# Performance work log

Hardware: AMD Instinct MI355X
Metric: run time of the kernel (lower is better)

## Reference

```python
import jax, jax.numpy as jnp
import numpy as np

B, C, H, W = 4, 512, 64, 64
WS = 32          # window size (square)
NHEADS = 8
GROUPS = 32      # GroupNorm groups (ldm Normalize)
EPS = 1e-6


def setup_inputs() -> dict:
    key = jax.random.key(0)
    ks = jax.random.split(key, 6)
    p = lambda k: jax.random.normal(k, (C, C), jnp.float32) * 0.02
    return {
        "x": jax.random.normal(ks[0], (B, C, H, W), jnp.float32),
        "norm_scale": jnp.ones((C,), jnp.float32),
        "norm_bias": jnp.zeros((C,), jnp.float32),
        "wq": p(ks[1]), "bq": jnp.zeros((C,), jnp.float32),
        "wk": p(ks[2]), "bk": jnp.zeros((C,), jnp.float32),
        "wv": p(ks[3]), "bv": jnp.zeros((C,), jnp.float32),
        "wo": p(ks[4]), "bo": jnp.zeros((C,), jnp.float32),
    }


def _group_norm(x, scale, bias):
    b, c, h, w = x.shape
    xg = x.reshape(b, GROUPS, c // GROUPS, h, w)
    mu = xg.mean(axis=(2, 3, 4), keepdims=True)
    var = ((xg - mu) ** 2).mean(axis=(2, 3, 4), keepdims=True)
    xn = ((xg - mu) * jax.lax.rsqrt(var + EPS)).reshape(b, c, h, w)
    return xn * scale[None, :, None, None] + bias[None, :, None, None]


def _conv1x1(t, w, b):
    return jnp.einsum('bchw,oc->bohw', t, w) + b[None, :, None, None]


def reference(x, norm_scale, norm_bias, wq, bq, wk, bk, wv, bv, wo, bo):
    b, c, hh, ww = x.shape
    h_ = _group_norm(x, norm_scale, norm_bias)

    # window partition: b c (h w1) (w w2) -> (b h w) c w1 w2  (H,W divisible by WS, no pad)
    nH, nW = hh // WS, ww // WS
    h_ = h_.reshape(b, c, nH, WS, nW, WS).transpose(0, 2, 4, 1, 3, 5)
    h_ = h_.reshape(b * nH * nW, c, WS, WS)

    q = _conv1x1(h_, wq, bq)
    k = _conv1x1(h_, wk, bk)
    v = _conv1x1(h_, wv, bv)

    bw = q.shape[0]
    n = WS * WS
    d = c // NHEADS

    def to_heads(t):  # b c h w -> b heads n d
        t = t.reshape(bw, c, n).transpose(0, 2, 1)          # b n c
        return t.reshape(bw, n, NHEADS, d).transpose(0, 2, 1, 3)

    q, k, v = map(to_heads, (q, k, v))

    scale = 1.0 / jnp.sqrt(jnp.asarray(d, q.dtype))
    scores = jnp.einsum('bhnd,bhmd->bhnm', q, k) * scale    # [bw, heads, n, n]
    attn = jax.nn.softmax(scores, axis=-1)
    out = jnp.einsum('bhnm,bhmd->bhnd', attn, v)
    out = out.transpose(0, 2, 1, 3).reshape(bw, n, c)       # b n c

    # window reverse: (b h w) (w1 w2) c -> b c (h w1) (w w2)
    out = out.reshape(b, nH, nW, WS, WS, c).transpose(0, 5, 1, 3, 2, 4)
    out = out.reshape(b, c, hh, ww)

    out = _conv1x1(out, wo, bo)
    return x + out
```

## Files before the change

kernel.cpp:

```cpp
#include <hip/hip_runtime.h>
#include <math.h>

typedef __bf16 bf16_t;
typedef bf16_t bf16x8 __attribute__((ext_vector_type(8)));
typedef float f32x16 __attribute__((ext_vector_type(16)));
typedef unsigned int u32x4 __attribute__((ext_vector_type(4)));

#define MFMA32(a, b, c) __builtin_amdgcn_mfma_f32_32x32x16_bf16(a, b, c, 0, 0, 0)
#define ROWOF(r, h) (((r) & 3) + 8 * ((r) >> 2) + 4 * (h))


static constexpr size_t OFF_STATS = 0;
static constexpr size_t OFF_W     = 4096;
static constexpr size_t OFF_HT    = OFF_W + 4u * 524288u;
static constexpr size_t OFF_Q     = OFF_HT + 16777216u;
static constexpr size_t OFF_K     = OFF_Q + 16777216u;
static constexpr size_t OFF_V     = OFF_K + 16777216u;
static constexpr size_t OFF_O     = OFF_HT;

__device__ __forceinline__ unsigned short f2bf(float f) {
  unsigned int u = __float_as_uint(f);
  u += 0x7fffu + ((u >> 16) & 1u);
  return (unsigned short)(u >> 16);
}

__global__ __launch_bounds__(256) void wconv_k(const float* __restrict__ w0, const float* __restrict__ w1,
                                               const float* __restrict__ w2, const float* __restrict__ w3,
                                               unsigned short* __restrict__ dst) {
  const float* srcs[4] = {w0, w1, w2, w3};
  const float* src = srcs[blockIdx.y];
  unsigned short* d = dst + (size_t)blockIdx.y * 262144u;
  int i = (blockIdx.x * 256 + threadIdx.x) * 4;
  float4 v = *(const float4*)(src + i);
  unsigned int lo = (unsigned int)f2bf(v.x) | ((unsigned int)f2bf(v.y) << 16);
  unsigned int hi = (unsigned int)f2bf(v.z) | ((unsigned int)f2bf(v.w) << 16);
  uint2 pk; pk.x = lo; pk.y = hi;
  *(uint2*)(d + i) = pk;
}

__global__ __launch_bounds__(256) void gn_stats_k(const float* __restrict__ x, float* __restrict__ stats) {
  int bg = blockIdx.x;
  const float* p = x + (size_t)bg * 65536u;
  int t = threadIdx.x;
  float s = 0.f, ss = 0.f;
  for (int i = t * 4; i < 65536; i += 1024) {
    float4 v = *(const float4*)(p + i);
    s += v.x + v.y + v.z + v.w;
    ss += v.x * v.x + v.y * v.y + v.z * v.z + v.w * v.w;
  }
  for (int m = 1; m <= 32; m <<= 1) { s += __shfl_xor(s, m); ss += __shfl_xor(ss, m); }
  __shared__ float rs[4], rss[4];
  int wv = t >> 6;
  if ((t & 63) == 0) { rs[wv] = s; rss[wv] = ss; }
  __syncthreads();
  if (t == 0) {
    s = rs[0] + rs[1] + rs[2] + rs[3];
    ss = rss[0] + rss[1] + rss[2] + rss[3];
    float mean = s * (1.f / 65536.f);
    float var = ss * (1.f / 65536.f) - mean * mean;
    stats[bg * 2] = mean;
    stats[bg * 2 + 1] = rsqrtf(var + 1e-6f);
  }
}

__global__ __launch_bounds__(256) void gn_apply_k(const float* __restrict__ x, const float* __restrict__ scale,
                                                  const float* __restrict__ bias, const float* __restrict__ stats,
                                                  unsigned short* __restrict__ ht) {
  __shared__ float tile[64][65];
  int blk = blockIdx.x;
  int b = blk >> 9, cblk = (blk >> 6) & 7, sblk = blk & 63;
  int c0 = cblk * 64, s0 = sblk * 64;
  int t = threadIdx.x;
#pragma unroll
  for (int p = 0; p < 4; ++p) {
    int i = p * 16 + (t >> 4);
    int j = (t & 15) * 4;
    int c = c0 + i;
    float mean = stats[(b * 32 + (c >> 4)) * 2];
    float rstd = stats[(b * 32 + (c >> 4)) * 2 + 1];
    float a = rstd * scale[c];
    float b2 = bias[c] - mean * a;
    float4 v = *(const float4*)(x + ((size_t)(b * 512 + c)) * 4096u + s0 + j);
    tile[i][j + 0] = v.x * a + b2;
    tile[i][j + 1] = v.y * a + b2;
    tile[i][j + 2] = v.z * a + b2;
    tile[i][j + 3] = v.w * a + b2;
  }
  __syncthreads();
#pragma unroll
  for (int p = 0; p < 8; ++p) {
    int jj = p * 8 + (t >> 5);
    int c2 = (t & 31) * 2;
    unsigned int pk = (unsigned int)f2bf(tile[c2][jj]) | ((unsigned int)f2bf(tile[c2 + 1][jj]) << 16);
    *(unsigned int*)(ht + ((size_t)b * 4096u + s0 + jj) * 512u + c0 + c2) = pk;
  }
}

__global__ __launch_bounds__(256, 2) void qkv_gemm_k(const unsigned short* __restrict__ wbf,
                                                     const unsigned short* __restrict__ ht,
                                                     const float* __restrict__ bq, const float* __restrict__ bk,
                                                     const float* __restrict__ bv,
                                                     unsigned short* __restrict__ Qatt,
                                                     unsigned short* __restrict__ Katt,
                                                     unsigned short* __restrict__ Vt) {
  int proj = blockIdx.z >> 2, b = blockIdx.z & 3;
  const unsigned short* W = wbf + (size_t)proj * 262144u;
  const float* biasp = (proj == 0) ? bq : (proj == 1) ? bk : bv;
  int o0 = blockIdx.x * 128, s0 = blockIdx.y * 128;
  __shared__ unsigned short Wl[128 * 72];
  __shared__ unsigned short Xl[128 * 72];
  int t = threadIdx.x, lane = t & 63, wv = t >> 6;
  int col_l = lane & 31, half = lane >> 5;
  int qm = (wv >> 1) * 64, qn = (wv & 1) * 64;
  f32x16 acc[2][2];
#pragma unroll
  for (int i = 0; i < 2; i++)
#pragma unroll
    for (int j = 0; j < 2; j++)
#pragma unroll
      for (int r = 0; r < 16; r++) acc[i][j][r] = 0.f;

  const unsigned short* hb = ht + ((size_t)b * 4096u + s0) * 512u;
  for (int kb = 0; kb < 512; kb += 64) {
    __syncthreads();
    {
      int row = t >> 3, ch = (t & 7) * 8;
#pragma unroll
      for (int p = 0; p < 4; ++p, row += 32) {
        *(uint4*)(Wl + row * 72 + ch) = *(const uint4*)(W + (size_t)(o0 + row) * 512u + kb + ch);
        *(uint4*)(Xl + row * 72 + ch) = *(const uint4*)(hb + (size_t)row * 512u + kb + ch);
      }
    }
    __syncthreads();
    const unsigned short* aT = (proj == 2) ? Wl : Xl;
    const unsigned short* bT = (proj == 2) ? Xl : Wl;
#pragma unroll
    for (int ks = 0; ks < 64; ks += 16) {
      bf16x8 a0 = *(const bf16x8*)(aT + (qm + col_l) * 72 + ks + 8 * half);
      bf16x8 a1 = *(const bf16x8*)(aT + (qm + 32 + col_l) * 72 + ks + 8 * half);
      bf16x8 b0 = *(const bf16x8*)(bT + (qn + col_l) * 72 + ks + 8 * half);
      bf16x8 b1 = *(const bf16x8*)(bT + (qn + 32 + col_l) * 72 + ks + 8 * half);
      acc[0][0] = MFMA32(a0, b0, acc[0][0]);
      acc[0][1] = MFMA32(a0, b1, acc[0][1]);
      acc[1][0] = MFMA32(a1, b0, acc[1][0]);
      acc[1][1] = MFMA32(a1, b1, acc[1][1]);
    }
  }

  if (proj <= 1) {
    unsigned short* dst = (proj == 0) ? Qatt : Katt;
#pragma unroll
    for (int i = 0; i < 2; i++)
#pragma unroll
      for (int j = 0; j < 2; j++) {
        int o = o0 + qn + 32 * j + col_l;
        int head = o >> 6, dd = o & 63;
        float bb = biasp[o];
#pragma unroll
        for (int r = 0; r < 16; r++) {
          int s = s0 + qm + 32 * i + ROWOF(r, half);
          int h = s >> 6, w = s & 63;
          int win = b * 4 + (h >> 5) * 2 + (w >> 5);
          int n = ((h & 31) << 5) | (w & 31);
          dst[(((size_t)(win * 8 + head)) * 1024u + n) * 64u + dd] = f2bf(acc[i][j][r] + bb);
        }
      }
  } else {
#pragma unroll
    for (int i = 0; i < 2; i++)
#pragma unroll
      for (int j = 0; j < 2; j++) {
        int s = s0 + qn + 32 * j + col_l;
        int h = s >> 6, w = s & 63;
        int win = b * 4 + (h >> 5) * 2 + (w >> 5);
        int n = ((h & 31) << 5) | (w & 31);
#pragma unroll
        for (int r = 0; r < 16; r++) {
          int o = o0 + qm + 32 * i + ROWOF(r, half);
          int head = o >> 6, dd = o & 63;
          Vt[(((size_t)(win * 8 + head)) * 64u + dd) * 1024u + n] = f2bf(acc[i][j][r] + biasp[o]);
        }
      }
  }
}

__global__ __launch_bounds__(256, 3) void attn_k(const unsigned short* __restrict__ Qatt,
                                                 const unsigned short* __restrict__ Katt,
                                                 const unsigned short* __restrict__ Vt,
                                                 unsigned short* __restrict__ Oimg) {
  int rb = blockIdx.x, head = blockIdx.y, win = blockIdx.z;
  int t = threadIdx.x, lane = t & 63, wv = t >> 6;
  int col_l = lane & 31, half = lane >> 5;
  __shared__ unsigned short Kl[128 * 72];
  __shared__ unsigned short Vl[64 * 136];
  const size_t wh = (size_t)(win * 8 + head);
  const unsigned short* Qb = Qatt + wh * 65536u;
  const unsigned short* Kb = Katt + wh * 65536u;
  const unsigned short* Vb = Vt + wh * 65536u;

  int qrow = rb * 128 + wv * 32 + col_l;
  bf16x8 qf[4];
#pragma unroll
  for (int kk = 0; kk < 4; kk++) qf[kk] = *(const bf16x8*)(Qb + (size_t)qrow * 64u + kk * 16 + 8 * half);

  f32x16 oacc[2];
#pragma unroll
  for (int j = 0; j < 2; j++)
#pragma unroll
    for (int r = 0; r < 16; r++) oacc[j][r] = 0.f;
  float lsum = 0.f;

  const float SC = 0.125f * 1.44269504f;

  for (int kt = 0; kt < 8; ++kt) {
    __syncthreads();
    {
      int row = t >> 3, ch = (t & 7) * 8;
#pragma unroll
      for (int p = 0; p < 4; ++p, row += 32)
        *(uint4*)(Kl + row * 72 + ch) = *(const uint4*)(Kb + ((size_t)(kt * 128 + row)) * 64u + ch);
      int vrow = t >> 4, vch = (t & 15) * 8;
#pragma unroll
      for (int p = 0; p < 4; ++p, vrow += 16)
        *(uint4*)(Vl + vrow * 136 + vch) = *(const uint4*)(Vb + (size_t)vrow * 1024u + kt * 128 + vch);
    }
    __syncthreads();

    f32x16 sacc[4];
#pragma unroll
    for (int jb = 0; jb < 4; jb++)
#pragma unroll
      for (int r = 0; r < 16; r++) sacc[jb][r] = 0.f;
#pragma unroll
    for (int jb = 0; jb < 4; jb++) {
#pragma unroll
      for (int kk = 0; kk < 4; kk++) {
        bf16x8 af = *(const bf16x8*)(Kl + (jb * 32 + col_l) * 72 + kk * 16 + 8 * half);
        sacc[jb] = MFMA32(af, qf[kk], sacc[jb]);
      }
    }

#pragma unroll
    for (int jb = 0; jb < 4; jb++) {
      float p[16];
#pragma unroll
      for (int r = 0; r < 16; r++) p[r] = __builtin_amdgcn_exp2f(sacc[jb][r] * SC);
      float ps = ((p[0] + p[1]) + (p[2] + p[3])) + ((p[4] + p[5]) + (p[6] + p[7]));
      ps += ((p[8] + p[9]) + (p[10] + p[11])) + ((p[12] + p[13]) + (p[14] + p[15]));
      lsum += ps;
      unsigned int pk[8];
#pragma unroll
      for (int j = 0; j < 8; j++)
        pk[j] = __builtin_amdgcn_perm(__float_as_uint(p[2 * j + 1]), __float_as_uint(p[2 * j]), 0x07060302u);
      unsigned int rA = __shfl_xor((int)(half ? pk[0] : pk[2]), 32);
      unsigned int rB = __shfl_xor((int)(half ? pk[1] : pk[3]), 32);
      unsigned int rC = __shfl_xor((int)(half ? pk[4] : pk[6]), 32);
      unsigned int rD = __shfl_xor((int)(half ? pk[5] : pk[7]), 32);
      u32x4 f0, f1;
      f0[0] = half ? rA : pk[0];
      f0[1] = half ? rB : pk[1];
      f0[2] = half ? pk[2] : rA;
      f0[3] = half ? pk[3] : rB;
      f1[0] = half ? rC : pk[4];
      f1[1] = half ? rD : pk[5];
      f1[2] = half ? pk[6] : rC;
      f1[3] = half ? pk[7] : rD;
      bf16x8 pa0 = __builtin_bit_cast(bf16x8, f0);
      bf16x8 pa1 = __builtin_bit_cast(bf16x8, f1);
#pragma unroll
      for (int dblk = 0; dblk < 2; dblk++) {
        bf16x8 v0 = *(const bf16x8*)(Vl + (dblk * 32 + col_l) * 136 + (jb * 2 + 0) * 16 + 8 * half);
        bf16x8 v1 = *(const bf16x8*)(Vl + (dblk * 32 + col_l) * 136 + (jb * 2 + 1) * 16 + 8 * half);
        oacc[dblk] = MFMA32(pa0, v0, oacc[dblk]);
        oacc[dblk] = MFMA32(pa1, v1, oacc[dblk]);
      }
    }
  }

  float l = lsum + __shfl_xor(lsum, 32);
  float inv = 1.f / l;

  int b = win >> 2, whn = (win >> 1) & 1, wwn = win & 1;
#pragma unroll
  for (int r = 0; r < 16; r++) {
    int qr = ROWOF(r, half);
    float invr = __shfl(inv, qr);
    int ntok = rb * 128 + wv * 32 + qr;
    int h = whn * 32 + (ntok >> 5), w = wwn * 32 + (ntok & 31);
    int s = h * 64 + w;
    size_t rowbase = ((size_t)b * 4096u + s) * 512u + head * 64;
    Oimg[rowbase + col_l] = f2bf(oacc[0][r] * invr);
    Oimg[rowbase + 32 + col_l] = f2bf(oacc[1][r] * invr);
  }
}

__global__ __launch_bounds__(256, 2) void out_gemm_k(const unsigned short* __restrict__ wo_bf,
                                                     const unsigned short* __restrict__ Oimg,
                                                     const float* __restrict__ bo, const float* __restrict__ x,
                                                     float* __restrict__ out) {
  int b = blockIdx.z;
  int o0 = blockIdx.x * 128, s0 = blockIdx.y * 128;
  __shared__ unsigned short Wl[128 * 72];
  __shared__ unsigned short Xl[128 * 72];
  int t = threadIdx.x, lane = t & 63, wv = t >> 6;
  int col_l = lane & 31, half = lane >> 5;
  int qm = (wv >> 1) * 64, qn = (wv & 1) * 64;
  f32x16 acc[2][2];
#pragma unroll
  for (int i = 0; i < 2; i++)
#pragma unroll
    for (int j = 0; j < 2; j++)
#pragma unroll
      for (int r = 0; r < 16; r++) acc[i][j][r] = 0.f;

  const unsigned short* ob = Oimg + ((size_t)b * 4096u + s0) * 512u;
  for (int kb = 0; kb < 512; kb += 64) {
    __syncthreads();
    {
      int row = t >> 3, ch = (t & 7) * 8;
#pragma unroll
      for (int p = 0; p < 4; ++p, row += 32) {
        *(uint4*)(Wl + row * 72 + ch) = *(const uint4*)(wo_bf + (size_t)(o0 + row) * 512u + kb + ch);
        *(uint4*)(Xl + row * 72 + ch) = *(const uint4*)(ob + (size_t)row * 512u + kb + ch);
      }
    }
    __syncthreads();
#pragma unroll
    for (int ks = 0; ks < 64; ks += 16) {
      bf16x8 a0 = *(const bf16x8*)(Wl + (qm + col_l) * 72 + ks + 8 * half);
      bf16x8 a1 = *(const bf16x8*)(Wl + (qm + 32 + col_l) * 72 + ks + 8 * half);
      bf16x8 b0 = *(const bf16x8*)(Xl + (qn + col_l) * 72 + ks + 8 * half);
      bf16x8 b1 = *(const bf16x8*)(Xl + (qn + 32 + col_l) * 72 + ks + 8 * half);
      acc[0][0] = MFMA32(a0, b0, acc[0][0]);
      acc[0][1] = MFMA32(a0, b1, acc[0][1]);
      acc[1][0] = MFMA32(a1, b0, acc[1][0]);
      acc[1][1] = MFMA32(a1, b1, acc[1][1]);
    }
  }
#pragma unroll
  for (int i = 0; i < 2; i++)
#pragma unroll
    for (int j = 0; j < 2; j++) {
      int s = s0 + qn + 32 * j + col_l;
#pragma unroll
      for (int r = 0; r < 16; r++) {
        int o = o0 + qm + 32 * i + ROWOF(r, half);
        size_t idx = ((size_t)b * 512u + o) * 4096u + s;
        out[idx] = x[idx] + acc[i][j][r] + bo[o];
      }
    }
}

extern "C" void kernel_launch(void* const* d_in, const int* in_sizes, int n_in,
                              void* d_out, int out_size, void* d_ws, size_t ws_size,
                              hipStream_t stream) {
  const float* x = (const float*)d_in[0];
  const float* nsc = (const float*)d_in[1];
  const float* nbi = (const float*)d_in[2];
  const float* wq = (const float*)d_in[3];
  const float* bq = (const float*)d_in[4];
  const float* wk = (const float*)d_in[5];
  const float* bk = (const float*)d_in[6];
  const float* wvp = (const float*)d_in[7];
  const float* bv = (const float*)d_in[8];
  const float* wo = (const float*)d_in[9];
  const float* bo = (const float*)d_in[10];
  float* out = (float*)d_out;
  char* ws = (char*)d_ws;

  float* stats = (float*)(ws + OFF_STATS);
  unsigned short* wbf = (unsigned short*)(ws + OFF_W);
  unsigned short* ht = (unsigned short*)(ws + OFF_HT);
  unsigned short* Qatt = (unsigned short*)(ws + OFF_Q);
  unsigned short* Katt = (unsigned short*)(ws + OFF_K);
  unsigned short* Vt = (unsigned short*)(ws + OFF_V);
  unsigned short* Oimg = (unsigned short*)(ws + OFF_O);

  wconv_k<<<dim3(256, 4), 256, 0, stream>>>(wq, wk, wvp, wo, wbf);
  gn_stats_k<<<128, 256, 0, stream>>>(x, stats);
  gn_apply_k<<<2048, 256, 0, stream>>>(x, nsc, nbi, stats, ht);
  qkv_gemm_k<<<dim3(4, 32, 12), 256, 0, stream>>>(wbf, ht, bq, bk, bv, Qatt, Katt, Vt);
  attn_k<<<dim3(8, 8, 16), 256, 0, stream>>>(Qatt, Katt, Vt, Oimg);
  out_gemm_k<<<dim3(4, 32, 4), 256, 0, stream>>>(wbf + 3u * 262144u, Oimg, bo, x, out);
}
```

Before: 281.6 us.

## Prefetch K/V tiles into registers and double-buffer LDS in attention kernel

The attention kernel now uses 512-thread blocks covering 256 query rows, which halves the number of blocks and doubles how much each staged K/V tile is reused. The next K/V tile is loaded into registers while the current tile is being computed, and shared memory is double-buffered so the global-load latency overlaps with the MFMA work. The grid is reordered so that blocks with the same window and head are adjacent, which may improve L2 locality. The cost is more shared memory and registers per block, plus an extra barrier per iteration.

```diff
diff --git a/kernel.cpp b/kernel.cpp
--- a/kernel.cpp
+++ b/kernel.cpp
@@ -184,24 +184,39 @@
   }
 }
 
-__global__ __launch_bounds__(256, 3) void attn_k(const unsigned short* __restrict__ Qatt,
+__global__ __launch_bounds__(512, 4) void attn_k(const unsigned short* __restrict__ Qatt,
                                                  const unsigned short* __restrict__ Katt,
                                                  const unsigned short* __restrict__ Vt,
                                                  unsigned short* __restrict__ Oimg) {
-  int rb = blockIdx.x, head = blockIdx.y, win = blockIdx.z;
+  int wh_idx = blockIdx.x, rb = blockIdx.y;
+  int win = wh_idx >> 3, head = wh_idx & 7;
   int t = threadIdx.x, lane = t & 63, wv = t >> 6;
   int col_l = lane & 31, half = lane >> 5;
-  __shared__ unsigned short Kl[128 * 72];
-  __shared__ unsigned short Vl[64 * 136];
-  const size_t wh = (size_t)(win * 8 + head);
+  __shared__ unsigned short Kl[2][128 * 72];
+  __shared__ unsigned short Vl[2][64 * 136];
+  const size_t wh = (size_t)wh_idx;
   const unsigned short* Qb = Qatt + wh * 65536u;
   const unsigned short* Kb = Katt + wh * 65536u;
   const unsigned short* Vb = Vt + wh * 65536u;
 
-  int qrow = rb * 128 + wv * 32 + col_l;
+  int qrow = rb * 256 + wv * 32 + col_l;
   bf16x8 qf[4];
 #pragma unroll
   for (int kk = 0; kk < 4; kk++) qf[kk] = *(const bf16x8*)(Qb + (size_t)qrow * 64u + kk * 16 + 8 * half);
+
+  int ki0 = t, ki1 = t + 512;
+  int krow0 = ki0 >> 3, kch0 = (ki0 & 7) * 8;
+  int krow1 = ki1 >> 3, kch1 = (ki1 & 7) * 8;
+  int vrow0 = ki0 >> 4, vch0 = (ki0 & 15) * 8;
+  int vrow1 = ki1 >> 4, vch1 = (ki1 & 15) * 8;
+
+  uint4 kr0, kr1, vr0, vr1;
+  {
+    kr0 = *(const uint4*)(Kb + (size_t)krow0 * 64u + kch0);
+    kr1 = *(const uint4*)(Kb + (size_t)krow1 * 64u + kch1);
+    vr0 = *(const uint4*)(Vb + (size_t)vrow0 * 1024u + vch0);
+    vr1 = *(const uint4*)(Vb + (size_t)vrow1 * 1024u + vch1);
+  }
 
   f32x16 oacc[2];
 #pragma unroll
@@ -213,18 +228,21 @@
   const float SC = 0.125f * 1.44269504f;
 
   for (int kt = 0; kt < 8; ++kt) {
-    __syncthreads();
-    {
-      int row = t >> 3, ch = (t & 7) * 8;
-#pragma unroll
-      for (int p = 0; p < 4; ++p, row += 32)
-        *(uint4*)(Kl + row * 72 + ch) = *(const uint4*)(Kb + ((size_t)(kt * 128 + row)) * 64u + ch);
-      int vrow = t >> 4, vch = (t & 15) * 8;
-#pragma unroll
-      for (int p = 0; p < 4; ++p, vrow += 16)
-        *(uint4*)(Vl + vrow * 136 + vch) = *(const uint4*)(Vb + (size_t)vrow * 1024u + kt * 128 + vch);
-    }
-    __syncthreads();
+    int buf = kt & 1;
+    unsigned short* Kc = Kl[buf];
+    unsigned short* Vc = Vl[buf];
+    *(uint4*)(Kc + krow0 * 72 + kch0) = kr0;
+    *(uint4*)(Kc + krow1 * 72 + kch1) = kr1;
+    *(uint4*)(Vc + vrow0 * 136 + vch0) = vr0;
+    *(uint4*)(Vc + vrow1 * 136 + vch1) = vr1;
+    __syncthreads();
+    if (kt < 7) {
+      int nk = (kt + 1) * 128;
+      kr0 = *(const uint4*)(Kb + (size_t)(nk + krow0) * 64u + kch0);
+      kr1 = *(const uint4*)(Kb + (size_t)(nk + krow1) * 64u + kch1);
+      vr0 = *(const uint4*)(Vb + (size_t)vrow0 * 1024u + nk + vch0);
+      vr1 = *(const uint4*)(Vb + (size_t)vrow1 * 1024u + nk + vch1);
+    }
 
     f32x16 sacc[4];
 #pragma unroll
@@ -235,7 +253,7 @@
     for (int jb = 0; jb < 4; jb++) {
 #pragma unroll
       for (int kk = 0; kk < 4; kk++) {
-        bf16x8 af = *(const bf16x8*)(Kl + (jb * 32 + col_l) * 72 + kk * 16 + 8 * half);
+        bf16x8 af = *(const bf16x8*)(Kc + (jb * 32 + col_l) * 72 + kk * 16 + 8 * half);
         sacc[jb] = MFMA32(af, qf[kk], sacc[jb]);
       }
     }
@@ -269,12 +287,13 @@
       bf16x8 pa1 = __builtin_bit_cast(bf16x8, f1);
 #pragma unroll
       for (int dblk = 0; dblk < 2; dblk++) {
-        bf16x8 v0 = *(const bf16x8*)(Vl + (dblk * 32 + col_l) * 136 + (jb * 2 + 0) * 16 + 8 * half);
-        bf16x8 v1 = *(const bf16x8*)(Vl + (dblk * 32 + col_l) * 136 + (jb * 2 + 1) * 16 + 8 * half);
+        bf16x8 v0 = *(const bf16x8*)(Vc + (dblk * 32 + col_l) * 136 + (jb * 2 + 0) * 16 + 8 * half);
+        bf16x8 v1 = *(const bf16x8*)(Vc + (dblk * 32 + col_l) * 136 + (jb * 2 + 1) * 16 + 8 * half);
         oacc[dblk] = MFMA32(pa0, v0, oacc[dblk]);
         oacc[dblk] = MFMA32(pa1, v1, oacc[dblk]);
       }
     }
+    __syncthreads();
   }
 
   float l = lsum + __shfl_xor(lsum, 32);
@@ -285,7 +304,7 @@
   for (int r = 0; r < 16; r++) {
     int qr = ROWOF(r, half);
     float invr = __shfl(inv, qr);
-    int ntok = rb * 128 + wv * 32 + qr;
+    int ntok = rb * 256 + wv * 32 + qr;
     int h = whn * 32 + (ntok >> 5), w = wwn * 32 + (ntok & 31);
     int s = h * 64 + w;
     size_t rowbase = ((size_t)b * 4096u + s) * 512u + head * 64;
@@ -380,6 +399,6 @@
   gn_stats_k<<<128, 256, 0, stream>>>(x, stats);
   gn_apply_k<<<2048, 256, 0, stream>>>(x, nsc, nbi, stats, ht);
   qkv_gemm_k<<<dim3(4, 32, 12), 256, 0, stream>>>(wbf, ht, bq, bk, bv, Qatt, Katt, Vt);
-  attn_k<<<dim3(8, 8, 16), 256, 0, stream>>>(Qatt, Katt, Vt, Oimg);
+  attn_k<<<dim3(128, 4), 512, 0, stream>>>(Qatt, Katt, Vt, Oimg);
   out_gemm_k<<<dim3(4, 32, 4), 256, 0, stream>>>(wbf + 3u * 262144u, Oimg, bo, x, out);
 }
```

Result: slower. 299.1 us (+6.2%).
